# Kernel optimization log

Hardware: AMD Instinct MI355X
Metric: run time of the kernel (lower is better)

Reference implementation:

```python
import jax, jax.numpy as jnp
import numpy as np

B, N, K = 8, 2048, 16   # batch, points, neighbors (after dropping self)
EPS = 1e-5


def _bn(y, g, b, m, v):
    # eval-mode batchnorm over channel dim 1, y: [B,C,...]
    sh = (1, -1) + (1,) * (y.ndim - 2)
    inv = g.reshape(sh) / jnp.sqrt(v.reshape(sh) + EPS)
    return (y - m.reshape(sh)) * inv + b.reshape(sh)


def setup_inputs() -> dict:
    key = jax.random.key(0)
    ks = jax.random.split(key, 16)
    d = {}
    d["x"] = jax.random.normal(ks[0], (B, 3, N), dtype=jnp.float32)
    # pre: Conv1d(3->24, k=1) + BN
    d["w_pre"] = jax.random.normal(ks[1], (24, 3), dtype=jnp.float32) * 0.3
    d["b_pre"] = jax.random.normal(ks[2], (24,), dtype=jnp.float32) * 0.1
    d["g_pre"] = 1.0 + 0.1 * jax.random.normal(ks[3], (24,), dtype=jnp.float32)
    d["be_pre"] = 0.1 * jax.random.normal(ks[4], (24,), dtype=jnp.float32)
    d["m_pre"] = 0.1 * jax.random.normal(ks[5], (24,), dtype=jnp.float32)
    d["v_pre"] = jax.random.uniform(ks[6], (24,), minval=0.5, maxval=1.5, dtype=jnp.float32)
    # shared_mlp_1: Conv2d(48->12, 1, bias=False) + BN
    d["w1"] = jax.random.normal(ks[7], (12, 48), dtype=jnp.float32) * 0.15
    d["g1"] = 1.0 + 0.1 * jax.random.normal(ks[8], (12,), dtype=jnp.float32)
    d["be1"] = 0.1 * jax.random.normal(ks[9], (12,), dtype=jnp.float32)
    d["m1"] = 0.1 * jax.random.normal(ks[10], (12,), dtype=jnp.float32)
    d["v1"] = jax.random.uniform(ks[11], (12,), minval=0.5, maxval=1.5, dtype=jnp.float32)
    # shared_mlp_2: Conv2d(60->12, 1, bias=False) + BN
    d["w2"] = jax.random.normal(ks[12], (12, 60), dtype=jnp.float32) * 0.15
    d["g2"] = 1.0 + 0.1 * jax.random.normal(ks[13], (12,), dtype=jnp.float32)
    d["be2"] = 0.1 * jax.random.normal(ks[14], (12,), dtype=jnp.float32)
    d["m2"] = 0.1 * jax.random.normal(ks[15], (12,), dtype=jnp.float32)
    d["v2"] = jnp.ones((12,), dtype=jnp.float32)
    # shared_mlp_3: Conv2d(72->12, 1, bias=False), no BN
    d["w3"] = jax.random.normal(jax.random.fold_in(key, 99), (12, 72), dtype=jnp.float32) * 0.15
    return d


def reference(x, w_pre, b_pre, g_pre, be_pre, m_pre, v_pre,
              w1, g1, be1, m1, v1, w2, g2, be2, m2, v2, w3):
    # pre: 1x1 conv1d + BN + ReLU -> [B,24,N]
    pre = jnp.einsum('oc,bcn->bon', w_pre, x) + b_pre[None, :, None]
    pre = jax.nn.relu(_bn(pre, g_pre, be_pre, m_pre, v_pre))

    # kNN on xyz = x.detach(): [B,N,3]
    pts = jax.lax.stop_gradient(jnp.swapaxes(x, 1, 2))
    sq = jnp.sum(pts * pts, axis=-1)                              # [B,N]
    d2 = sq[:, :, None] + sq[:, None, :] - 2.0 * jnp.einsum('bnc,bmc->bnm', pts, pts)
    _, idx = jax.lax.top_k(-d2, K + 1)                             # nearest K+1 incl. self
    idx = idx[..., 1:]                                             # drop self -> [B,N,K]

    # gather neighbor features: [B,24,N,K]
    grouped = jax.vmap(lambda f, i: f[:, i])(pre, idx)
    center = jnp.broadcast_to(pre[..., None], grouped.shape)
    y = jnp.concatenate([center, grouped], axis=1)                 # [B,48,N,K]

    h1 = jax.nn.relu(_bn(jnp.einsum('oc,bcnk->bonk', w1, y), g1, be1, m1, v1))
    y = jnp.concatenate([h1, y], axis=1)                           # [B,60,N,K]
    h2 = jax.nn.relu(_bn(jnp.einsum('oc,bcnk->bonk', w2, y), g2, be2, m2, v2))
    y = jnp.concatenate([h2, y], axis=1)                           # [B,72,N,K]
    h3 = jnp.einsum('oc,bcnk->bonk', w3, y)
    y = jnp.concatenate([h3, y], axis=1)                           # [B,84,N,K]

    y = jnp.max(y, axis=-1)                                        # maxpool over neighbors -> [B,84,N]
    return jnp.concatenate([y, x], axis=1)                         # [B,87,N]
```

## Files before the change

### kernel.cpp

```cpp
#include <hip/hip_runtime.h>
#include <math.h>

#define EPS 1e-5f
#define NBATCH 8
#define NPTS 2048
#define KNB 16
#define BIG 3.2e38f

#define CHUNK_PTS 32
#define KNN_BLKS (NBATCH * 64)
#define THREADS 512
#define FUSED_LDS 49152

#define WS_PRE 0
#define WS_AUX (16384 * 24)
#define WS_IDX (WS_AUX + 16384 * 72)

__device__ __forceinline__ float dist2f(float mex, float mey, float mez,
                                        float sqn, float4 q) {
  float dot2 = fmaf(mex, q.x, fmaf(mey, q.y, __fmul_rn(mez, q.z)));
  return __fsub_rn(__fadd_rn(sqn, q.w), dot2);
}

template <bool HASSELF>
__device__ __forceinline__ void scan_slice(const float4* __restrict__ Cs, int selfc,
                                           float mex, float mey, float mez,
                                           float sqn, float L[16]) {
  for (int c0 = 0; c0 < 128; c0 += 16) {
    float S[16];
#pragma unroll
    for (int cc = 0; cc < 16; ++cc) {
      float4 q = Cs[c0 + cc];
      float d2 = dist2f(mex, mey, mez, sqn, q);
      if (HASSELF) S[cc] = ((c0 + cc) == selfc) ? BIG : d2;
      else         S[cc] = d2;
    }
#pragma unroll
    for (int pw = 1; pw < 16; pw <<= 1) {
#pragma unroll
      for (int k = pw; k >= 1; k >>= 1) {
#pragma unroll
        for (int j = (k & (pw - 1)); j + k < 16; j += 2 * k) {
#pragma unroll
          for (int i = 0; i < k; ++i) {
            int a = i + j, bq = i + j + k;
            if (bq < 16 && (a / (2 * pw) == bq / (2 * pw))) {
              float lo = fminf(S[a], S[bq]);
              float hi = fmaxf(S[a], S[bq]);
              S[a] = lo; S[bq] = hi;
            }
          }
        }
      }
    }
    float m[16];
#pragma unroll
    for (int i = 0; i < 16; ++i) m[i] = fminf(L[i], S[15 - i]);
#pragma unroll
    for (int d = 8; d >= 1; d >>= 1) {
#pragma unroll
      for (int i = 0; i < 16; ++i) {
        if (!(i & d)) {
          float lo = fminf(m[i], m[i | d]);
          float hi = fmaxf(m[i], m[i | d]);
          m[i] = lo; m[i | d] = hi;
        }
      }
    }
#pragma unroll
    for (int i = 0; i < 16; ++i) L[i] = m[i];
  }
}

__global__ __launch_bounds__(THREADS, 6) void fused_kernel(
    const float* __restrict__ x,
    const float* __restrict__ w_pre, const float* __restrict__ b_pre,
    const float* __restrict__ g_pre, const float* __restrict__ be_pre,
    const float* __restrict__ m_pre, const float* __restrict__ v_pre,
    const float* __restrict__ w1, const float* __restrict__ g1,
    const float* __restrict__ be1, const float* __restrict__ m1,
    const float* __restrict__ v1,
    const float* __restrict__ w2, const float* __restrict__ g2,
    const float* __restrict__ be2, const float* __restrict__ m2,
    const float* __restrict__ v2, const float* __restrict__ w3,
    float* __restrict__ pre, float* __restrict__ aux,
    int* __restrict__ knn_out) {
  extern __shared__ char smem[];
  float4* C4   = (float4*)smem;
  float* slist = (float*)(smem + 32768);
  float* fwp   = slist;
  float* fbp   = fwp + 72;
  float* fw1t  = fbp + 24;
  float* fb1   = fw1t + 576;
  float* fw2t  = fb1 + 12;
  float* fb2   = fw2t + 720;
  float* fw3t  = fb2 + 12;
  float* sinv1 = fw3t + 576;
  float* sinv2 = sinv1 + 12;
  float* sinvP = sinv2 + 12;
  float* sd2  = slist;
  int*   sidx = (int*)(slist + 640);
  int*   scnt = (int*)(slist + 1280);

  int tid = threadIdx.x;
  int bi = blockIdx.x;
  int b = bi >> 6, chunk = bi & 63;
  const float* xb = x + (size_t)b * 3 * NPTS;

  for (int j = tid; j < NPTS; j += THREADS) {
    float xx = xb[j], yy = xb[NPTS + j], zz = xb[2 * NPTS + j];
    float sq = __fadd_rn(__fadd_rn(__fmul_rn(xx, xx), __fmul_rn(yy, yy)),
                         __fmul_rn(zz, zz));
    C4[j] = make_float4(2.0f * xx, 2.0f * yy, 2.0f * zz, sq);
  }
  if (tid < 24) sinvP[tid] = g_pre[tid] / sqrtf(v_pre[tid] + EPS);
  if (tid < 12) { sinv1[tid] = g1[tid] / sqrtf(v1[tid] + EPS);
                  sinv2[tid] = g2[tid] / sqrtf(v2[tid] + EPS); }
  __syncthreads();
  if (tid < 72) fwp[tid] = w_pre[tid] * sinvP[tid / 3];
  if (tid < 24) fbp[tid] = (b_pre[tid] - m_pre[tid]) * sinvP[tid] + be_pre[tid];
  if (tid < 12) { fb1[tid] = be1[tid] - m1[tid] * sinv1[tid];
                  fb2[tid] = be2[tid] - m2[tid] * sinv2[tid]; }
  for (int j = tid; j < 576; j += THREADS) { int i = j / 12, o = j - i * 12; fw1t[j] = w1[o * 48 + i] * sinv1[o]; }
  for (int j = tid; j < 720; j += THREADS) { int i = j / 12, o = j - i * 12; fw2t[j] = w2[o * 60 + i] * sinv2[o]; }
  for (int j = tid; j < 576; j += THREADS) { int i = j / 12, o = j - i * 12; fw3t[j] = w3[o * 72 + 24 + i]; }
  __syncthreads();

  {
    int r = tid & 15, pt = tid >> 4;
    int n0 = chunk * CHUNK_PTS + pt;
    size_t pgl = (size_t)(b << 11) + n0;
    float x0 = xb[n0], x1 = xb[NPTS + n0], x2 = xb[2 * NPTS + n0];
    float pr[24];
#pragma unroll
    for (int c = 0; c < 24; ++c) {
      float v = fmaf(fwp[c * 3 + 0], x0,
                fmaf(fwp[c * 3 + 1], x1,
                fmaf(fwp[c * 3 + 2], x2, fbp[c])));
      pr[c] = fmaxf(v, 0.f);
    }
    if (r == 12) {
      float4* o4 = (float4*)(pre + pgl * 24);
#pragma unroll
      for (int i = 0; i < 6; ++i)
        o4[i] = make_float4(pr[4*i], pr[4*i+1], pr[4*i+2], pr[4*i+3]);
    }
    if (r < 12) {
      int o = r;
      float u1 = fb1[o], a1 = 0.f, u2 = fb2[o], a2 = 0.f, u3 = 0.f, a3 = 0.f;
#pragma unroll
      for (int i = 0; i < 24; ++i) {
        u1 = fmaf(fw1t[i * 12 + o],        pr[i], u1);
        a1 = fmaf(fw1t[(24 + i) * 12 + o], pr[i], a1);
        u2 = fmaf(fw2t[(12 + i) * 12 + o], pr[i], u2);
        a2 = fmaf(fw2t[(36 + i) * 12 + o], pr[i], a2);
        u3 = fmaf(fw3t[i * 12 + o],        pr[i], u3);
        a3 = fmaf(fw3t[(24 + i) * 12 + o], pr[i], a3);
      }
      float* A = aux + pgl * 72;
      A[o] = u1; A[12 + o] = u2; A[24 + o] = u3;
      A[36 + o] = a1; A[48 + o] = a2; A[60 + o] = a3;
    }
  }
  __syncthreads();

  int p = tid & 31, s = tid >> 5;
  int w = tid >> 6;
  int n = chunk * CHUNK_PTS + p;
  float4 me4 = C4[n];
  float mex = 0.5f * me4.x, mey = 0.5f * me4.y, mez = 0.5f * me4.z;
  float sqn = me4.w;
  const float4* Cs = C4 + s * 128;
  int selfc = n - s * 128;
  int wself = chunk >> 3;
  float L[16];
#pragma unroll
  for (int t = 0; t < 16; ++t) L[t] = BIG;
  if (w == wself) scan_slice<true >(Cs, selfc, mex, mey, mez, sqn, L);
  else            scan_slice<false>(Cs, selfc, mex, mey, mez, sqn, L);
  {
    float bb[16], m16[16];
#pragma unroll
    for (int i = 0; i < 16; ++i) bb[i] = __shfl_xor(L[i], 32, 64);
#pragma unroll
    for (int i = 0; i < 16; ++i) m16[i] = fminf(L[i], bb[15 - i]);
#pragma unroll
    for (int d = 8; d >= 1; d >>= 1) {
#pragma unroll
      for (int i = 0; i < 16; ++i) {
        if (!(i & d)) {
          float lo = fminf(m16[i], m16[i | d]);
          float hi = fmaxf(m16[i], m16[i | d]);
          m16[i] = lo; m16[i | d] = hi;
        }
      }
    }
    if (!(s & 1)) {
#pragma unroll
      for (int i = 0; i < 16; ++i) slist[(w * 16 + i) * 32 + p] = m16[i];
    }
  }
  __syncthreads();
  for (int W = 4; W >= 1; W >>= 1) {
    int u = tid >> 5;
    bool act = (u < W);
    float a[16], bb[16];
    if (act) {
#pragma unroll
      for (int i = 0; i < 16; ++i) a[i]  = slist[((2 * u) * 16 + i) * 32 + p];
#pragma unroll
      for (int i = 0; i < 16; ++i) bb[i] = slist[((2 * u + 1) * 16 + i) * 32 + p];
    }
    __syncthreads();
    if (act) {
      float m16[16];
#pragma unroll
      for (int i = 0; i < 16; ++i) m16[i] = fminf(a[i], bb[15 - i]);
#pragma unroll
      for (int d = 8; d >= 1; d >>= 1) {
#pragma unroll
        for (int i = 0; i < 16; ++i) {
          if (!(i & d)) {
            float lo = fminf(m16[i], m16[i | d]);
            float hi = fmaxf(m16[i], m16[i | d]);
            m16[i] = lo; m16[i | d] = hi;
          }
        }
      }
#pragma unroll
      for (int i = 0; i < 16; ++i) slist[(u * 16 + i) * 32 + p] = m16[i];
    }
    __syncthreads();
  }
  float tau = slist[15 * 32 + p];
  __syncthreads();
  for (int j = tid; j < 32 * 20; j += THREADS) sidx[j] = 0;
  if (tid < 32) scnt[tid] = 0;
  __syncthreads();
  if (w == wself) {
#pragma unroll 4
    for (int c = 0; c < 128; ++c) {
      float4 q = Cs[c];
      float d2 = dist2f(mex, mey, mez, sqn, q);
      int j = s * 128 + c;
      if (d2 <= tau && j != n) {
        int pos = atomicAdd(&scnt[p], 1);
        if (pos < 20) { sd2[p * 20 + pos] = d2; sidx[p * 20 + pos] = j; }
      }
    }
  } else {
#pragma unroll 4
    for (int c = 0; c < 128; ++c) {
      float4 q = Cs[c];
      float d2 = dist2f(mex, mey, mez, sqn, q);
      int j = s * 128 + c;
      if (d2 <= tau) {
        int pos = atomicAdd(&scnt[p], 1);
        if (pos < 20) { sd2[p * 20 + pos] = d2; sidx[p * 20 + pos] = j; }
      }
    }
  }
  __syncthreads();
  if (tid < 32) {
    int c = scnt[tid]; if (c > 20) c = 20;
    if (c > 16) {
      for (int t = 0; t < 16; ++t) {
        int best = t;
        for (int u = t + 1; u < c; ++u) {
          float da = sd2[tid * 20 + u], db = sd2[tid * 20 + best];
          int ia = sidx[tid * 20 + u], ib = sidx[tid * 20 + best];
          if (da < db || (da == db && ia < ib)) best = u;
        }
        float td = sd2[tid * 20 + t]; sd2[tid * 20 + t] = sd2[tid * 20 + best]; sd2[tid * 20 + best] = td;
        int ti = sidx[tid * 20 + t]; sidx[tid * 20 + t] = sidx[tid * 20 + best]; sidx[tid * 20 + best] = ti;
      }
    }
  }
  __syncthreads();
  {
    int pp = tid >> 4, kk = tid & 15;
    knn_out[((size_t)b * NPTS + chunk * CHUNK_PTS + pp) * KNB + kk] = sidx[pp * 20 + kk];
  }
}

__global__ __launch_bounds__(256) void mlp_kernel(
    const float* __restrict__ pre, const float* __restrict__ aux,
    const int* __restrict__ knn, const float* __restrict__ x,
    const float* __restrict__ w2, const float* __restrict__ g2,
    const float* __restrict__ v2, const float* __restrict__ w3,
    float* __restrict__ out) {
  __shared__ float sW2h[144], sW3h2[144], sW3h1[144];
  __shared__ float sout[87 * 16];
  int tid = threadIdx.x;
  if (tid < 144) {
    int o = tid / 12, i = tid - o * 12;
    float inv2 = g2[o] / sqrtf(v2[o] + EPS);
    sW2h[tid]  = w2[o * 60 + i] * inv2;
    sW3h2[tid] = w3[o * 72 + i];
    sW3h1[tid] = w3[o * 72 + 12 + i];
  }
  __syncthreads();
  int k = tid & 15, pl = tid >> 4;
  int p = blockIdx.x * 16 + pl;
  int b = p >> 11, n = p & (NPTS - 1);
  int nb = knn[(size_t)p * KNB + k];
  const float4* u4 = (const float4*)(aux + (size_t)p * 72);
  const float4* a4 = (const float4*)(aux + ((size_t)(b << 11) + nb) * 72 + 36);
  float uc[36], av[36];
#pragma unroll
  for (int i = 0; i < 9; ++i) {
    float4 t = u4[i];
    uc[4*i] = t.x; uc[4*i+1] = t.y; uc[4*i+2] = t.z; uc[4*i+3] = t.w;
    float4 t2 = a4[i];
    av[4*i] = t2.x; av[4*i+1] = t2.y; av[4*i+2] = t2.z; av[4*i+3] = t2.w;
  }
  float h1[12], h2[12], h3[12];
#pragma unroll
  for (int o = 0; o < 12; ++o) h1[o] = fmaxf(uc[o] + av[o], 0.f);
#pragma unroll
  for (int o = 0; o < 12; ++o) {
    float a = uc[12 + o] + av[12 + o];
#pragma unroll
    for (int i = 0; i < 12; ++i) a = fmaf(sW2h[o * 12 + i], h1[i], a);
    h2[o] = fmaxf(a, 0.f);
  }
#pragma unroll
  for (int o = 0; o < 12; ++o) {
    float a = uc[24 + o] + av[24 + o];
#pragma unroll
    for (int i = 0; i < 12; ++i) a = fmaf(sW3h2[o * 12 + i], h2[i], a);
#pragma unroll
    for (int i = 0; i < 12; ++i) a = fmaf(sW3h1[o * 12 + i], h1[i], a);
    h3[o] = a;
  }
  float nbf[24];
  const float4* pn4 = (const float4*)(pre + ((size_t)(b << 11) + nb) * 24);
#pragma unroll
  for (int i = 0; i < 6; ++i) {
    float4 t = pn4[i];
    nbf[4*i] = t.x; nbf[4*i+1] = t.y; nbf[4*i+2] = t.z; nbf[4*i+3] = t.w;
  }
#pragma unroll
  for (int m = 1; m < 16; m <<= 1) {
#pragma unroll
    for (int o = 0; o < 12; ++o) {
      h1[o] = fmaxf(h1[o], __shfl_xor(h1[o], m, 16));
      h2[o] = fmaxf(h2[o], __shfl_xor(h2[o], m, 16));
      h3[o] = fmaxf(h3[o], __shfl_xor(h3[o], m, 16));
    }
#pragma unroll
    for (int i = 0; i < 24; ++i)
      nbf[i] = fmaxf(nbf[i], __shfl_xor(nbf[i], m, 16));
  }
  if (k == 0) {
    const float4* c4 = (const float4*)(pre + (size_t)p * 24);
#pragma unroll
    for (int o = 0; o < 12; ++o) {
      sout[(0  + o) * 16 + pl] = h3[o];
      sout[(12 + o) * 16 + pl] = h2[o];
      sout[(24 + o) * 16 + pl] = h1[o];
    }
#pragma unroll
    for (int i = 0; i < 6; ++i) {
      float4 t = c4[i];
      sout[(36 + 4*i    ) * 16 + pl] = t.x;
      sout[(36 + 4*i + 1) * 16 + pl] = t.y;
      sout[(36 + 4*i + 2) * 16 + pl] = t.z;
      sout[(36 + 4*i + 3) * 16 + pl] = t.w;
    }
#pragma unroll
    for (int i = 0; i < 24; ++i) sout[(60 + i) * 16 + pl] = nbf[i];
    const float* xb = x + (size_t)b * 3 * NPTS + n;
    sout[84 * 16 + pl] = xb[0];
    sout[85 * 16 + pl] = xb[NPTS];
    sout[86 * 16 + pl] = xb[2 * NPTS];
  }
  __syncthreads();
  int n0 = (blockIdx.x * 16) & (NPTS - 1);
  float* ob = out + (size_t)b * 87 * NPTS;
  for (int j2 = tid; j2 < 87 * 16; j2 += 256) {
    int c = j2 >> 4, i = j2 & 15;
    ob[(size_t)c * NPTS + n0 + i] = sout[j2];
  }
}

extern "C" void kernel_launch(void* const* d_in, const int* in_sizes, int n_in,
                              void* d_out, int out_size, void* d_ws, size_t ws_size,
                              hipStream_t stream) {
  (void)in_sizes; (void)n_in; (void)out_size; (void)ws_size;
  const float* x     = (const float*)d_in[0];
  const float* w_pre = (const float*)d_in[1];
  const float* b_pre = (const float*)d_in[2];
  const float* g_pre = (const float*)d_in[3];
  const float* be_pre= (const float*)d_in[4];
  const float* m_pre = (const float*)d_in[5];
  const float* v_pre = (const float*)d_in[6];
  const float* w1    = (const float*)d_in[7];
  const float* g1    = (const float*)d_in[8];
  const float* be1   = (const float*)d_in[9];
  const float* m1    = (const float*)d_in[10];
  const float* v1    = (const float*)d_in[11];
  const float* w2    = (const float*)d_in[12];
  const float* g2    = (const float*)d_in[13];
  const float* be2   = (const float*)d_in[14];
  const float* m2    = (const float*)d_in[15];
  const float* v2    = (const float*)d_in[16];
  const float* w3    = (const float*)d_in[17];
  float* ws  = (float*)d_ws;
  float* pre = ws + WS_PRE;
  float* aux = ws + WS_AUX;
  int*   knn = (int*)(ws + WS_IDX);
  float* out = (float*)d_out;

  fused_kernel<<<KNN_BLKS, THREADS, FUSED_LDS, stream>>>(
      x, w_pre, b_pre, g_pre, be_pre, m_pre, v_pre,
      w1, g1, be1, m1, v1, w2, g2, be2, m2, v2, w3,
      pre, aux, knn);
  mlp_kernel<<<NBATCH * NPTS / 16, 256, 0, stream>>>(pre, aux, knn, x,
                                                     w2, g2, v2, w3, out);
}
```

Before: 151.5 us.

## Halve KNN block to 16 points, add in-wave two-level merge and LDS swizzle

Shrinks each fused block from 32 points with 512 threads to 16 points with 256 threads, doubling the grid so that more blocks run concurrently. The first stage of the top-16 merge now uses two in-wave shuffle steps (xor 16, then xor 32) instead of an LDS round trip. Each group of 16 threads reads the candidate slice in an XOR-rotated order, which spreads broadcast LDS reads across banks. The distance is rewritten with negated coordinates so it becomes a single FMA chain, which can change rounding slightly relative to the reference. The work in the unseen later part of the kernel must still match the new chunk size.

```diff
diff --git a/kernel.cpp b/kernel.cpp
--- a/kernel.cpp
+++ b/kernel.cpp
@@ -7,10 +7,10 @@
 #define KNB 16
 #define BIG 3.2e38f
 
-#define CHUNK_PTS 32
-#define KNN_BLKS (NBATCH * 64)
-#define THREADS 512
-#define FUSED_LDS 49152
+#define CHUNK_PTS 16
+#define KNN_BLKS (NBATCH * 128)
+#define THREADS 256
+#define FUSED_LDS 40960
 
 #define WS_PRE 0
 #define WS_AUX (16384 * 24)
@@ -18,21 +18,21 @@
 
 __device__ __forceinline__ float dist2f(float mex, float mey, float mez,
                                         float sqn, float4 q) {
-  float dot2 = fmaf(mex, q.x, fmaf(mey, q.y, __fmul_rn(mez, q.z)));
-  return __fsub_rn(__fadd_rn(sqn, q.w), dot2);
+  return fmaf(mex, q.x, fmaf(mey, q.y, fmaf(mez, q.z, __fadd_rn(sqn, q.w))));
 }
 
 template <bool HASSELF>
 __device__ __forceinline__ void scan_slice(const float4* __restrict__ Cs, int selfc,
-                                           float mex, float mey, float mez,
+                                           int rot, float mex, float mey, float mez,
                                            float sqn, float L[16]) {
   for (int c0 = 0; c0 < 128; c0 += 16) {
     float S[16];
 #pragma unroll
     for (int cc = 0; cc < 16; ++cc) {
-      float4 q = Cs[c0 + cc];
+      int c2 = (c0 + cc) ^ rot;
+      float4 q = Cs[c2];
       float d2 = dist2f(mex, mey, mez, sqn, q);
-      if (HASSELF) S[cc] = ((c0 + cc) == selfc) ? BIG : d2;
+      if (HASSELF) S[cc] = (c2 == selfc) ? BIG : d2;
       else         S[cc] = d2;
     }
 #pragma unroll
@@ -72,7 +72,7 @@
   }
 }
 
-__global__ __launch_bounds__(THREADS, 6) void fused_kernel(
+__global__ __launch_bounds__(THREADS, 4) void fused_kernel(
     const float* __restrict__ x,
     const float* __restrict__ w_pre, const float* __restrict__ b_pre,
     const float* __restrict__ g_pre, const float* __restrict__ be_pre,
@@ -99,19 +99,19 @@
   float* sinv2 = sinv1 + 12;
   float* sinvP = sinv2 + 12;
   float* sd2  = slist;
-  int*   sidx = (int*)(slist + 640);
-  int*   scnt = (int*)(slist + 1280);
+  int*   sidx = (int*)(slist + 320);
+  int*   scnt = (int*)(slist + 640);
 
   int tid = threadIdx.x;
   int bi = blockIdx.x;
-  int b = bi >> 6, chunk = bi & 63;
+  int b = bi >> 7, chunk = bi & 127;
   const float* xb = x + (size_t)b * 3 * NPTS;
 
   for (int j = tid; j < NPTS; j += THREADS) {
     float xx = xb[j], yy = xb[NPTS + j], zz = xb[2 * NPTS + j];
     float sq = __fadd_rn(__fadd_rn(__fmul_rn(xx, xx), __fmul_rn(yy, yy)),
                          __fmul_rn(zz, zz));
-    C4[j] = make_float4(2.0f * xx, 2.0f * yy, 2.0f * zz, sq);
+    C4[j] = make_float4(-2.0f * xx, -2.0f * yy, -2.0f * zz, sq);
   }
   if (tid < 24) sinvP[tid] = g_pre[tid] / sqrtf(v_pre[tid] + EPS);
   if (tid < 12) { sinv1[tid] = g1[tid] / sqrtf(v1[tid] + EPS);
@@ -164,24 +164,25 @@
   }
   __syncthreads();
 
-  int p = tid & 31, s = tid >> 5;
+  int p = tid & 15, s = tid >> 4;
   int w = tid >> 6;
   int n = chunk * CHUNK_PTS + p;
   float4 me4 = C4[n];
-  float mex = 0.5f * me4.x, mey = 0.5f * me4.y, mez = 0.5f * me4.z;
+  float mex = -0.5f * me4.x, mey = -0.5f * me4.y, mez = -0.5f * me4.z;
   float sqn = me4.w;
   const float4* Cs = C4 + s * 128;
   int selfc = n - s * 128;
-  int wself = chunk >> 3;
+  int rot = (s & 3) << 1;
+  int wself = chunk >> 5;
   float L[16];
 #pragma unroll
   for (int t = 0; t < 16; ++t) L[t] = BIG;
-  if (w == wself) scan_slice<true >(Cs, selfc, mex, mey, mez, sqn, L);
-  else            scan_slice<false>(Cs, selfc, mex, mey, mez, sqn, L);
+  if (w == wself) scan_slice<true >(Cs, selfc, rot, mex, mey, mez, sqn, L);
+  else            scan_slice<false>(Cs, selfc, rot, mex, mey, mez, sqn, L);
   {
     float bb[16], m16[16];
 #pragma unroll
-    for (int i = 0; i < 16; ++i) bb[i] = __shfl_xor(L[i], 32, 64);
+    for (int i = 0; i < 16; ++i) bb[i] = __shfl_xor(L[i], 16, 64);
 #pragma unroll
     for (int i = 0; i < 16; ++i) m16[i] = fminf(L[i], bb[15 - i]);
 #pragma unroll
@@ -195,21 +196,37 @@
         }
       }
     }
-    if (!(s & 1)) {
-#pragma unroll
-      for (int i = 0; i < 16; ++i) slist[(w * 16 + i) * 32 + p] = m16[i];
-    }
-  }
-  __syncthreads();
-  for (int W = 4; W >= 1; W >>= 1) {
-    int u = tid >> 5;
+#pragma unroll
+    for (int i = 0; i < 16; ++i) bb[i] = __shfl_xor(m16[i], 32, 64);
+    float m2_[16];
+#pragma unroll
+    for (int i = 0; i < 16; ++i) m2_[i] = fminf(m16[i], bb[15 - i]);
+#pragma unroll
+    for (int d = 8; d >= 1; d >>= 1) {
+#pragma unroll
+      for (int i = 0; i < 16; ++i) {
+        if (!(i & d)) {
+          float lo = fminf(m2_[i], m2_[i | d]);
+          float hi = fmaxf(m2_[i], m2_[i | d]);
+          m2_[i] = lo; m2_[i | d] = hi;
+        }
+      }
+    }
+    if ((s & 3) == 0) {
+#pragma unroll
+      for (int i = 0; i < 16; ++i) slist[(w * 16 + i) * 16 + p] = m2_[i];
+    }
+  }
+  __syncthreads();
+  for (int W = 2; W >= 1; W >>= 1) {
+    int u = tid >> 4;
     bool act = (u < W);
     float a[16], bb[16];
     if (act) {
 #pragma unroll
-      for (int i = 0; i < 16; ++i) a[i]  = slist[((2 * u) * 16 + i) * 32 + p];
-#pragma unroll
-      for (int i = 0; i < 16; ++i) bb[i] = slist[((2 * u + 1) * 16 + i) * 32 + p];
+      for (int i = 0; i < 16; ++i) a[i]  = slist[((2 * u) * 16 + i) * 16 + p];
+#pragma unroll
+      for (int i = 0; i < 16; ++i) bb[i] = slist[((2 * u + 1) * 16 + i) * 16 + p];
     }
     __syncthreads();
     if (act) {
@@ -228,21 +245,22 @@
         }
       }
 #pragma unroll
-      for (int i = 0; i < 16; ++i) slist[(u * 16 + i) * 32 + p] = m16[i];
+      for (int i = 0; i < 16; ++i) slist[(u * 16 + i) * 16 + p] = m16[i];
     }
     __syncthreads();
   }
-  float tau = slist[15 * 32 + p];
-  __syncthreads();
-  for (int j = tid; j < 32 * 20; j += THREADS) sidx[j] = 0;
-  if (tid < 32) scnt[tid] = 0;
+  float tau = slist[15 * 16 + p];
+  __syncthreads();
+  for (int j = tid; j < 16 * 20; j += THREADS) sidx[j] = 0;
+  if (tid < 16) scnt[tid] = 0;
   __syncthreads();
   if (w == wself) {
 #pragma unroll 4
     for (int c = 0; c < 128; ++c) {
-      float4 q = Cs[c];
+      int c2 = c ^ rot;
+      float4 q = Cs[c2];
       float d2 = dist2f(mex, mey, mez, sqn, q);
-      int j = s * 128 + c;
+      int j = s * 128 + c2;
       if (d2 <= tau && j != n) {
         int pos = atomicAdd(&scnt[p], 1);
         if (pos < 20) { sd2[p * 20 + pos] = d2; sidx[p * 20 + pos] = j; }
@@ -251,9 +269,10 @@
   } else {
 #pragma unroll 4
     for (int c = 0; c < 128; ++c) {
-      float4 q = Cs[c];
+      int c2 = c ^ rot;
+      float4 q = Cs[c2];
       float d2 = dist2f(mex, mey, mez, sqn, q);
-      int j = s * 128 + c;
+      int j = s * 128 + c2;
       if (d2 <= tau) {
         int pos = atomicAdd(&scnt[p], 1);
         if (pos < 20) { sd2[p * 20 + pos] = d2; sidx[p * 20 + pos] = j; }
@@ -261,7 +280,7 @@
     }
   }
   __syncthreads();
-  if (tid < 32) {
+  if (tid < 16) {
     int c = scnt[tid]; if (c > 20) c = 20;
     if (c > 16) {
       for (int t = 0; t < 16; ++t) {
```

Result: slower. 158.6 us (+4.7%).

## Remap KNN threads so top-16 merge happens within a wavefront via shuffles

Applied to the files above, without the earlier changes.

Threads are remapped so each wavefront owns 4 query points across 16 candidate slices, letting the per-point top-16 merge run entirely through xor-shuffles instead of a multi-round LDS tree reduction with several block barriers. The self-exclusion template split is removed and the distance is folded into a single fma chain using negated coordinates. Scratch buffers get their own LDS region, so their zeroing moves earlier and the LDS size shrinks. Launch bounds drop from 6 to 4 blocks per CU, which gives more registers per thread but may lower occupancy; removing the barrier after the MLP stage relies on the new LDS layout not overlapping the weights.

```diff
diff --git a/kernel.cpp b/kernel.cpp
--- a/kernel.cpp
+++ b/kernel.cpp
@@ -10,7 +10,7 @@
 #define CHUNK_PTS 32
 #define KNN_BLKS (NBATCH * 64)
 #define THREADS 512
-#define FUSED_LDS 49152
+#define FUSED_LDS 46176
 
 #define WS_PRE 0
 #define WS_AUX (16384 * 24)
@@ -18,61 +18,10 @@
 
 __device__ __forceinline__ float dist2f(float mex, float mey, float mez,
                                         float sqn, float4 q) {
-  float dot2 = fmaf(mex, q.x, fmaf(mey, q.y, __fmul_rn(mez, q.z)));
-  return __fsub_rn(__fadd_rn(sqn, q.w), dot2);
+  return fmaf(mex, q.x, fmaf(mey, q.y, fmaf(mez, q.z, __fadd_rn(sqn, q.w))));
 }
 
-template <bool HASSELF>
-__device__ __forceinline__ void scan_slice(const float4* __restrict__ Cs, int selfc,
-                                           float mex, float mey, float mez,
-                                           float sqn, float L[16]) {
-  for (int c0 = 0; c0 < 128; c0 += 16) {
-    float S[16];
-#pragma unroll
-    for (int cc = 0; cc < 16; ++cc) {
-      float4 q = Cs[c0 + cc];
-      float d2 = dist2f(mex, mey, mez, sqn, q);
-      if (HASSELF) S[cc] = ((c0 + cc) == selfc) ? BIG : d2;
-      else         S[cc] = d2;
-    }
-#pragma unroll
-    for (int pw = 1; pw < 16; pw <<= 1) {
-#pragma unroll
-      for (int k = pw; k >= 1; k >>= 1) {
-#pragma unroll
-        for (int j = (k & (pw - 1)); j + k < 16; j += 2 * k) {
-#pragma unroll
-          for (int i = 0; i < k; ++i) {
-            int a = i + j, bq = i + j + k;
-            if (bq < 16 && (a / (2 * pw) == bq / (2 * pw))) {
-              float lo = fminf(S[a], S[bq]);
-              float hi = fmaxf(S[a], S[bq]);
-              S[a] = lo; S[bq] = hi;
-            }
-          }
-        }
-      }
-    }
-    float m[16];
-#pragma unroll
-    for (int i = 0; i < 16; ++i) m[i] = fminf(L[i], S[15 - i]);
-#pragma unroll
-    for (int d = 8; d >= 1; d >>= 1) {
-#pragma unroll
-      for (int i = 0; i < 16; ++i) {
-        if (!(i & d)) {
-          float lo = fminf(m[i], m[i | d]);
-          float hi = fmaxf(m[i], m[i | d]);
-          m[i] = lo; m[i | d] = hi;
-        }
-      }
-    }
-#pragma unroll
-    for (int i = 0; i < 16; ++i) L[i] = m[i];
-  }
-}
-
-__global__ __launch_bounds__(THREADS, 6) void fused_kernel(
+__global__ __launch_bounds__(THREADS, 4) void fused_kernel(
     const float* __restrict__ x,
     const float* __restrict__ w_pre, const float* __restrict__ b_pre,
     const float* __restrict__ g_pre, const float* __restrict__ be_pre,
@@ -86,9 +35,9 @@
     float* __restrict__ pre, float* __restrict__ aux,
     int* __restrict__ knn_out) {
   extern __shared__ char smem[];
-  float4* C4   = (float4*)smem;
-  float* slist = (float*)(smem + 32768);
-  float* fwp   = slist;
+  float4* C4  = (float4*)smem;
+  float* wreg = (float*)(smem + 32768);
+  float* fwp   = wreg;
   float* fbp   = fwp + 72;
   float* fw1t  = fbp + 24;
   float* fb1   = fw1t + 576;
@@ -98,9 +47,9 @@
   float* sinv1 = fw3t + 576;
   float* sinv2 = sinv1 + 12;
   float* sinvP = sinv2 + 12;
-  float* sd2  = slist;
-  int*   sidx = (int*)(slist + 640);
-  int*   scnt = (int*)(slist + 1280);
+  float* sd2  = (float*)(smem + 40928);
+  int*   sidx = (int*)(smem + 43488);
+  int*   scnt = (int*)(smem + 46048);
 
   int tid = threadIdx.x;
   int bi = blockIdx.x;
@@ -111,8 +60,10 @@
     float xx = xb[j], yy = xb[NPTS + j], zz = xb[2 * NPTS + j];
     float sq = __fadd_rn(__fadd_rn(__fmul_rn(xx, xx), __fmul_rn(yy, yy)),
                          __fmul_rn(zz, zz));
-    C4[j] = make_float4(2.0f * xx, 2.0f * yy, 2.0f * zz, sq);
-  }
+    C4[j] = make_float4(-2.0f * xx, -2.0f * yy, -2.0f * zz, sq);
+  }
+  for (int j = tid; j < 32 * 20; j += THREADS) sidx[j] = 0;
+  if (tid < 32) scnt[tid] = 0;
   if (tid < 24) sinvP[tid] = g_pre[tid] / sqrtf(v_pre[tid] + EPS);
   if (tid < 12) { sinv1[tid] = g1[tid] / sqrtf(v1[tid] + EPS);
                   sinv2[tid] = g2[tid] / sqrtf(v2[tid] + EPS); }
@@ -162,26 +113,68 @@
       A[36 + o] = a1; A[48 + o] = a2; A[60 + o] = a3;
     }
   }
-  __syncthreads();
-
-  int p = tid & 31, s = tid >> 5;
+
+  int l = tid & 63;
   int w = tid >> 6;
+  int p = (w << 2) | (l & 3);
+  int s = l >> 2;
   int n = chunk * CHUNK_PTS + p;
   float4 me4 = C4[n];
-  float mex = 0.5f * me4.x, mey = 0.5f * me4.y, mez = 0.5f * me4.z;
+  float mex = -0.5f * me4.x, mey = -0.5f * me4.y, mez = -0.5f * me4.z;
   float sqn = me4.w;
   const float4* Cs = C4 + s * 128;
   int selfc = n - s * 128;
-  int wself = chunk >> 3;
   float L[16];
 #pragma unroll
   for (int t = 0; t < 16; ++t) L[t] = BIG;
-  if (w == wself) scan_slice<true >(Cs, selfc, mex, mey, mez, sqn, L);
-  else            scan_slice<false>(Cs, selfc, mex, mey, mez, sqn, L);
-  {
+  for (int c0 = 0; c0 < 128; c0 += 16) {
+    float S[16];
+#pragma unroll
+    for (int cc = 0; cc < 16; ++cc) {
+      float4 q = Cs[c0 + cc];
+      float d2 = dist2f(mex, mey, mez, sqn, q);
+      S[cc] = ((c0 + cc) == selfc) ? BIG : d2;
+    }
+#pragma unroll
+    for (int pw = 1; pw < 16; pw <<= 1) {
+#pragma unroll
+      for (int k = pw; k >= 1; k >>= 1) {
+#pragma unroll
+        for (int j = (k & (pw - 1)); j + k < 16; j += 2 * k) {
+#pragma unroll
+          for (int i = 0; i < k; ++i) {
+            int a = i + j, bq = i + j + k;
+            if (bq < 16 && (a / (2 * pw) == bq / (2 * pw))) {
+              float lo = fminf(S[a], S[bq]);
+              float hi = fmaxf(S[a], S[bq]);
+              S[a] = lo; S[bq] = hi;
+            }
+          }
+        }
+      }
+    }
+    float m[16];
+#pragma unroll
+    for (int i = 0; i < 16; ++i) m[i] = fminf(L[i], S[15 - i]);
+#pragma unroll
+    for (int d = 8; d >= 1; d >>= 1) {
+#pragma unroll
+      for (int i = 0; i < 16; ++i) {
+        if (!(i & d)) {
+          float lo = fminf(m[i], m[i | d]);
+          float hi = fmaxf(m[i], m[i | d]);
+          m[i] = lo; m[i | d] = hi;
+        }
+      }
+    }
+#pragma unroll
+    for (int i = 0; i < 16; ++i) L[i] = m[i];
+  }
+#pragma unroll
+  for (int mk = 4; mk <= 32; mk <<= 1) {
     float bb[16], m16[16];
 #pragma unroll
-    for (int i = 0; i < 16; ++i) bb[i] = __shfl_xor(L[i], 32, 64);
+    for (int i = 0; i < 16; ++i) bb[i] = __shfl_xor(L[i], mk, 64);
 #pragma unroll
     for (int i = 0; i < 16; ++i) m16[i] = fminf(L[i], bb[15 - i]);
 #pragma unroll
@@ -195,69 +188,18 @@
         }
       }
     }
-    if (!(s & 1)) {
-#pragma unroll
-      for (int i = 0; i < 16; ++i) slist[(w * 16 + i) * 32 + p] = m16[i];
-    }
-  }
-  __syncthreads();
-  for (int W = 4; W >= 1; W >>= 1) {
-    int u = tid >> 5;
-    bool act = (u < W);
-    float a[16], bb[16];
-    if (act) {
-#pragma unroll
-      for (int i = 0; i < 16; ++i) a[i]  = slist[((2 * u) * 16 + i) * 32 + p];
-#pragma unroll
-      for (int i = 0; i < 16; ++i) bb[i] = slist[((2 * u + 1) * 16 + i) * 32 + p];
-    }
-    __syncthreads();
-    if (act) {
-      float m16[16];
-#pragma unroll
-      for (int i = 0; i < 16; ++i) m16[i] = fminf(a[i], bb[15 - i]);
-#pragma unroll
-      for (int d = 8; d >= 1; d >>= 1) {
-#pragma unroll
-        for (int i = 0; i < 16; ++i) {
-          if (!(i & d)) {
-            float lo = fminf(m16[i], m16[i | d]);
-            float hi = fmaxf(m16[i], m16[i | d]);
-            m16[i] = lo; m16[i | d] = hi;
-          }
-        }
-      }
-#pragma unroll
-      for (int i = 0; i < 16; ++i) slist[(u * 16 + i) * 32 + p] = m16[i];
-    }
-    __syncthreads();
-  }
-  float tau = slist[15 * 32 + p];
-  __syncthreads();
-  for (int j = tid; j < 32 * 20; j += THREADS) sidx[j] = 0;
-  if (tid < 32) scnt[tid] = 0;
-  __syncthreads();
-  if (w == wself) {
+#pragma unroll
+    for (int i = 0; i < 16; ++i) L[i] = m16[i];
+  }
+  float tau = L[15];
 #pragma unroll 4
-    for (int c = 0; c < 128; ++c) {
-      float4 q = Cs[c];
-      float d2 = dist2f(mex, mey, mez, sqn, q);
-      int j = s * 128 + c;
-      if (d2 <= tau && j != n) {
-        int pos = atomicAdd(&scnt[p], 1);
-        if (pos < 20) { sd2[p * 20 + pos] = d2; sidx[p * 20 + pos] = j; }
-      }
-    }
-  } else {
-#pragma unroll 4
-    for (int c = 0; c < 128; ++c) {
-      float4 q = Cs[c];
-      float d2 = dist2f(mex, mey, mez, sqn, q);
-      int j = s * 128 + c;
-      if (d2 <= tau) {
-        int pos = atomicAdd(&scnt[p], 1);
-        if (pos < 20) { sd2[p * 20 + pos] = d2; sidx[p * 20 + pos] = j; }
-      }
+  for (int c = 0; c < 128; ++c) {
+    float4 q = Cs[c];
+    float d2 = dist2f(mex, mey, mez, sqn, q);
+    int j = s * 128 + c;
+    if (d2 <= tau && j != n) {
+      int pos = atomicAdd(&scnt[p], 1);
+      if (pos < 20) { sd2[p * 20 + pos] = d2; sidx[p * 20 + pos] = j; }
     }
   }
   __syncthreads();
```

Result: slower. 159.9 us (+5.5%).

## Sort points by x and search KNN in a local window with fallback

Applied to the files above, without the earlier changes.

A new kernel bitonic-sorts each batch's points by x coordinate. The KNN kernel then scans only a window of 768 sorted neighbours around each query instead of all 2048 points. It checks whether the x-gap to the window edges could hide a closer point and, if so, falls back to the full scan from global memory. This cuts distance computations and shared-memory footprint, at the cost of an extra sort launch, a mapping of indices back to original order, and a slower path for blocks that need the fallback.

```diff
diff --git a/kernel.cpp b/kernel.cpp
--- a/kernel.cpp
+++ b/kernel.cpp
@@ -10,65 +10,103 @@
 #define CHUNK_PTS 32
 #define KNN_BLKS (NBATCH * 64)
 #define THREADS 512
-#define FUSED_LDS 49152
+#define HALF 384
+#define WMAX 832
+#define FUSED_LDS 38304
 
 #define WS_PRE 0
-#define WS_AUX (16384 * 24)
-#define WS_IDX (WS_AUX + 16384 * 72)
-
-__device__ __forceinline__ float dist2f(float mex, float mey, float mez,
-                                        float sqn, float4 q) {
-  float dot2 = fmaf(mex, q.x, fmaf(mey, q.y, __fmul_rn(mez, q.z)));
-  return __fsub_rn(__fadd_rn(sqn, q.w), dot2);
-}
-
-template <bool HASSELF>
-__device__ __forceinline__ void scan_slice(const float4* __restrict__ Cs, int selfc,
-                                           float mex, float mey, float mez,
-                                           float sqn, float L[16]) {
-  for (int c0 = 0; c0 < 128; c0 += 16) {
-    float S[16];
-#pragma unroll
-    for (int cc = 0; cc < 16; ++cc) {
-      float4 q = Cs[c0 + cc];
-      float d2 = dist2f(mex, mey, mez, sqn, q);
-      if (HASSELF) S[cc] = ((c0 + cc) == selfc) ? BIG : d2;
-      else         S[cc] = d2;
-    }
-#pragma unroll
-    for (int pw = 1; pw < 16; pw <<= 1) {
-#pragma unroll
-      for (int k = pw; k >= 1; k >>= 1) {
-#pragma unroll
-        for (int j = (k & (pw - 1)); j + k < 16; j += 2 * k) {
-#pragma unroll
-          for (int i = 0; i < k; ++i) {
-            int a = i + j, bq = i + j + k;
-            if (bq < 16 && (a / (2 * pw) == bq / (2 * pw))) {
-              float lo = fminf(S[a], S[bq]);
-              float hi = fmaxf(S[a], S[bq]);
-              S[a] = lo; S[bq] = hi;
-            }
+#define WS_AUX 393216
+#define WS_IDX 1572864
+#define WS_SX4 1835008
+#define WS_SID 1900544
+
+__device__ __forceinline__ float dist2f(float mex, float mey, float mez, float sqn,
+                                        float qx, float qy, float qz, float qw) {
+  return fmaf(mex, qx, fmaf(mey, qy, fmaf(mez, qz, __fadd_rn(sqn, qw))));
+}
+
+__device__ __forceinline__ void sort16(float S[16]) {
+#pragma unroll
+  for (int pw = 1; pw < 16; pw <<= 1) {
+#pragma unroll
+    for (int k = pw; k >= 1; k >>= 1) {
+#pragma unroll
+      for (int j = (k & (pw - 1)); j + k < 16; j += 2 * k) {
+#pragma unroll
+        for (int i = 0; i < k; ++i) {
+          int a = i + j, bq = i + j + k;
+          if (bq < 16 && (a / (2 * pw) == bq / (2 * pw))) {
+            float lo = fminf(S[a], S[bq]);
+            float hi = fmaxf(S[a], S[bq]);
+            S[a] = lo; S[bq] = hi;
           }
         }
       }
     }
-    float m[16];
-#pragma unroll
-    for (int i = 0; i < 16; ++i) m[i] = fminf(L[i], S[15 - i]);
-#pragma unroll
-    for (int d = 8; d >= 1; d >>= 1) {
-#pragma unroll
-      for (int i = 0; i < 16; ++i) {
-        if (!(i & d)) {
-          float lo = fminf(m[i], m[i | d]);
-          float hi = fmaxf(m[i], m[i | d]);
-          m[i] = lo; m[i | d] = hi;
-        }
-      }
-    }
-#pragma unroll
-    for (int i = 0; i < 16; ++i) L[i] = m[i];
+  }
+}
+
+__device__ __forceinline__ void clean16(float m[16]) {
+#pragma unroll
+  for (int d = 8; d >= 1; d >>= 1) {
+#pragma unroll
+    for (int i = 0; i < 16; ++i) {
+      if (!(i & d)) {
+        float lo = fminf(m[i], m[i | d]);
+        float hi = fmaxf(m[i], m[i | d]);
+        m[i] = lo; m[i | d] = hi;
+      }
+    }
+  }
+}
+
+__device__ __forceinline__ void merge16(float L[16], const float S[16]) {
+  float m[16];
+#pragma unroll
+  for (int i = 0; i < 16; ++i) m[i] = fminf(L[i], S[15 - i]);
+  clean16(m);
+#pragma unroll
+  for (int i = 0; i < 16; ++i) L[i] = m[i];
+}
+
+__device__ __forceinline__ void shflmerge16(float L[16], int mask) {
+  float bb[16], m[16];
+#pragma unroll
+  for (int i = 0; i < 16; ++i) bb[i] = __shfl_xor(L[i], mask, 64);
+#pragma unroll
+  for (int i = 0; i < 16; ++i) m[i] = fminf(L[i], bb[15 - i]);
+  clean16(m);
+#pragma unroll
+  for (int i = 0; i < 16; ++i) L[i] = m[i];
+}
+
+__global__ __launch_bounds__(1024) void sort_kernel(
+    const float* __restrict__ x, float* __restrict__ sx4g, int* __restrict__ sidxg) {
+  __shared__ float kx[NPTS];
+  __shared__ int ki[NPTS];
+  int b = blockIdx.x, tid = threadIdx.x;
+  const float* xb = x + (size_t)b * 3 * NPTS;
+  for (int j = tid; j < NPTS; j += 1024) { kx[j] = xb[j]; ki[j] = j; }
+  __syncthreads();
+  for (int k = 2; k <= NPTS; k <<= 1) {
+    for (int j = k >> 1; j > 0; j >>= 1) {
+      int t = 2 * tid - (tid & (j - 1));
+      int t2 = t | j;
+      bool up = ((t & k) == 0);
+      float a = kx[t], c = kx[t2];
+      int ia = ki[t], ic = ki[t2];
+      bool sw = up ? (a > c) : (a < c);
+      if (sw) { kx[t] = c; kx[t2] = a; ki[t] = ic; ki[t2] = ia; }
+      __syncthreads();
+    }
+  }
+  for (int j = tid; j < NPTS; j += 1024) {
+    int n = ki[j];
+    float xx = kx[j], yy = xb[NPTS + n], zz = xb[2 * NPTS + n];
+    float sq = __fadd_rn(__fadd_rn(__fmul_rn(xx, xx), __fmul_rn(yy, yy)),
+                         __fmul_rn(zz, zz));
+    ((float4*)sx4g)[(b << 11) + j] = make_float4(-2.0f * xx, -2.0f * yy, -2.0f * zz, sq);
+    sidxg[(b << 11) + j] = n;
   }
 }
 
@@ -83,12 +121,14 @@
     const float* __restrict__ w2, const float* __restrict__ g2,
     const float* __restrict__ be2, const float* __restrict__ m2,
     const float* __restrict__ v2, const float* __restrict__ w3,
+    const float* __restrict__ sx4g, const int* __restrict__ sidxg,
     float* __restrict__ pre, float* __restrict__ aux,
     int* __restrict__ knn_out) {
   extern __shared__ char smem[];
-  float4* C4   = (float4*)smem;
-  float* slist = (float*)(smem + 32768);
-  float* fwp   = slist;
+  float2* Wxy = (float2*)smem;
+  float2* Wzs = (float2*)(smem + 6656);
+  int*   Widx = (int*)(smem + 13312);
+  float* fwp   = (float*)(smem + 16640);
   float* fbp   = fwp + 72;
   float* fw1t  = fbp + 24;
   float* fb1   = fw1t + 576;
@@ -98,21 +138,36 @@
   float* sinv1 = fw3t + 576;
   float* sinv2 = sinv1 + 12;
   float* sinvP = sinv2 + 12;
-  float* sd2  = slist;
-  int*   sidx = (int*)(slist + 640);
-  int*   scnt = (int*)(slist + 1280);
+  float* slist = (float*)(smem + 16640);
+  float* sd2   = (float*)(smem + 33024);
+  int*   sidxT = (int*)(smem + 35584);
+  int*   scnt  = (int*)(smem + 38144);
+  int*   sflag = (int*)(smem + 38272);
 
   int tid = threadIdx.x;
   int bi = blockIdx.x;
   int b = bi >> 6, chunk = bi & 63;
+  int bq = b << 11;
+  int vlo = chunk * CHUNK_PTS - HALF;
   const float* xb = x + (size_t)b * 3 * NPTS;
-
-  for (int j = tid; j < NPTS; j += THREADS) {
-    float xx = xb[j], yy = xb[NPTS + j], zz = xb[2 * NPTS + j];
-    float sq = __fadd_rn(__fadd_rn(__fmul_rn(xx, xx), __fmul_rn(yy, yy)),
-                         __fmul_rn(zz, zz));
-    C4[j] = make_float4(2.0f * xx, 2.0f * yy, 2.0f * zz, sq);
-  }
+  const float4* sx4 = (const float4*)sx4g;
+
+  for (int idx = tid; idx < WMAX; idx += THREADS) {
+    int g = vlo + idx;
+    if ((unsigned)g < (unsigned)NPTS) {
+      float4 f = sx4[bq + g];
+      Wxy[idx] = make_float2(f.x, f.y);
+      Wzs[idx] = make_float2(f.z, f.w);
+      Widx[idx] = sidxg[bq + g];
+    } else {
+      Wxy[idx] = make_float2(0.f, 0.f);
+      Wzs[idx] = make_float2(0.f, BIG);
+      Widx[idx] = 0;
+    }
+  }
+  for (int j = tid; j < 32 * 20; j += THREADS) sidxT[j] = 0;
+  if (tid < 32) scnt[tid] = 0;
+  if (tid == 32) *sflag = 0;
   if (tid < 24) sinvP[tid] = g_pre[tid] / sqrtf(v_pre[tid] + EPS);
   if (tid < 12) { sinv1[tid] = g1[tid] / sqrtf(v1[tid] + EPS);
                   sinv2[tid] = g2[tid] / sqrtf(v2[tid] + EPS); }
@@ -128,8 +183,8 @@
 
   {
     int r = tid & 15, pt = tid >> 4;
-    int n0 = chunk * CHUNK_PTS + pt;
-    size_t pgl = (size_t)(b << 11) + n0;
+    int n0 = sidxg[bq + chunk * CHUNK_PTS + pt];
+    size_t pgl = (size_t)bq + n0;
     float x0 = xb[n0], x1 = xb[NPTS + n0], x2 = xb[2 * NPTS + n0];
     float pr[24];
 #pragma unroll
@@ -165,40 +220,32 @@
   __syncthreads();
 
   int p = tid & 31, s = tid >> 5;
-  int w = tid >> 6;
-  int n = chunk * CHUNK_PTS + p;
-  float4 me4 = C4[n];
-  float mex = 0.5f * me4.x, mey = 0.5f * me4.y, mez = 0.5f * me4.z;
-  float sqn = me4.w;
-  const float4* Cs = C4 + s * 128;
-  int selfc = n - s * 128;
-  int wself = chunk >> 3;
+  int q = chunk * CHUNK_PTS + p;
+  float2 mxy = Wxy[p + HALF], mzs = Wzs[p + HALF];
+  float mex = -0.5f * mxy.x, mey = -0.5f * mxy.y, mez = -0.5f * mzs.x;
+  float sqn = mzs.y;
   float L[16];
 #pragma unroll
   for (int t = 0; t < 16; ++t) L[t] = BIG;
-  if (w == wself) scan_slice<true >(Cs, selfc, mex, mey, mez, sqn, L);
-  else            scan_slice<false>(Cs, selfc, mex, mey, mez, sqn, L);
-  {
-    float bb[16], m16[16];
-#pragma unroll
-    for (int i = 0; i < 16; ++i) bb[i] = __shfl_xor(L[i], 32, 64);
-#pragma unroll
-    for (int i = 0; i < 16; ++i) m16[i] = fminf(L[i], bb[15 - i]);
-#pragma unroll
-    for (int d = 8; d >= 1; d >>= 1) {
-#pragma unroll
-      for (int i = 0; i < 16; ++i) {
-        if (!(i & d)) {
-          float lo = fminf(m16[i], m16[i | d]);
-          float hi = fmaxf(m16[i], m16[i | d]);
-          m16[i] = lo; m16[i | d] = hi;
-        }
-      }
-    }
-    if (!(s & 1)) {
-#pragma unroll
-      for (int i = 0; i < 16; ++i) slist[(w * 16 + i) * 32 + p] = m16[i];
-    }
+#pragma unroll
+  for (int t = 0; t < 3; ++t) {
+    float S[16];
+#pragma unroll
+    for (int cc = 0; cc < 16; ++cc) {
+      int idx = p + s * 16 + t * 256 + cc;
+      float2 a = Wxy[idx], z = Wzs[idx];
+      float d2 = dist2f(mex, mey, mez, sqn, a.x, a.y, z.x, z.y);
+      if (t * 256 + cc == 256) d2 = (s == 8) ? BIG : d2;
+      S[cc] = d2;
+    }
+    sort16(S);
+    merge16(L, S);
+  }
+  shflmerge16(L, 32);
+  if (!(s & 1)) {
+    int w = tid >> 6;
+#pragma unroll
+    for (int i = 0; i < 16; ++i) slist[(w * 16 + i) * 32 + p] = L[i];
   }
   __syncthreads();
   for (int W = 4; W >= 1; W >>= 1) {
@@ -213,50 +260,98 @@
     }
     __syncthreads();
     if (act) {
-      float m16[16];
-#pragma unroll
-      for (int i = 0; i < 16; ++i) m16[i] = fminf(a[i], bb[15 - i]);
-#pragma unroll
-      for (int d = 8; d >= 1; d >>= 1) {
-#pragma unroll
-        for (int i = 0; i < 16; ++i) {
-          if (!(i & d)) {
-            float lo = fminf(m16[i], m16[i | d]);
-            float hi = fmaxf(m16[i], m16[i | d]);
-            m16[i] = lo; m16[i | d] = hi;
-          }
+      float m[16];
+#pragma unroll
+      for (int i = 0; i < 16; ++i) m[i] = fminf(a[i], bb[15 - i]);
+      clean16(m);
+#pragma unroll
+      for (int i = 0; i < 16; ++i) slist[(u * 16 + i) * 32 + p] = m[i];
+    }
+    __syncthreads();
+  }
+  float tau = slist[15 * 32 + p];
+  if (tid < 32) {
+    int qq = chunk * CHUNK_PTS + tid;
+    float xq = -0.5f * Wxy[tid + HALF].x;
+    float tt = slist[15 * 32 + tid];
+    bool bad = false;
+    int gl = qq - HALF - 1;
+    if (gl >= 0) { float xe = -0.5f * sx4[bq + gl].x; float dx = xe - xq; if (dx * dx <= tt) bad = true; }
+    int gr = qq + HALF;
+    if (gr < NPTS) { float xe = -0.5f * sx4[bq + gr].x; float dx = xe - xq; if (dx * dx <= tt) bad = true; }
+    if (bad) atomicOr(sflag, 1);
+  }
+  __syncthreads();
+  int flag = *sflag;
+
+  if (!flag) {
+#pragma unroll
+    for (int t = 0; t < 3; ++t) {
+#pragma unroll
+      for (int cc = 0; cc < 16; ++cc) {
+        int idx = p + s * 16 + t * 256 + cc;
+        float2 a = Wxy[idx], z = Wzs[idx];
+        float d2 = dist2f(mex, mey, mez, sqn, a.x, a.y, z.x, z.y);
+        bool self = (t * 256 + cc == 256) && (s == 8);
+        if (!self && d2 <= tau) {
+          int pos = atomicAdd(&scnt[p], 1);
+          if (pos < 20) { sd2[p * 20 + pos] = d2; sidxT[p * 20 + pos] = Widx[idx]; }
         }
       }
-#pragma unroll
-      for (int i = 0; i < 16; ++i) slist[(u * 16 + i) * 32 + p] = m16[i];
+    }
+  } else {
+    const float4* Cg = sx4 + bq + s * 128;
+    float L2[16];
+#pragma unroll
+    for (int t = 0; t < 16; ++t) L2[t] = BIG;
+    for (int c0 = 0; c0 < 128; c0 += 16) {
+      float S[16];
+#pragma unroll
+      for (int cc = 0; cc < 16; ++cc) {
+        float4 f = Cg[c0 + cc];
+        float d2 = dist2f(mex, mey, mez, sqn, f.x, f.y, f.z, f.w);
+        int gg = s * 128 + c0 + cc;
+        S[cc] = (gg == q) ? BIG : d2;
+      }
+      sort16(S);
+      merge16(L2, S);
+    }
+    shflmerge16(L2, 32);
+    if (!(s & 1)) {
+      int w = tid >> 6;
+#pragma unroll
+      for (int i = 0; i < 16; ++i) slist[(w * 16 + i) * 32 + p] = L2[i];
     }
     __syncthreads();
-  }
-  float tau = slist[15 * 32 + p];
-  __syncthreads();
-  for (int j = tid; j < 32 * 20; j += THREADS) sidx[j] = 0;
-  if (tid < 32) scnt[tid] = 0;
-  __syncthreads();
-  if (w == wself) {
-#pragma unroll 4
+    for (int W = 4; W >= 1; W >>= 1) {
+      int u = tid >> 5;
+      bool act = (u < W);
+      float a[16], bb[16];
+      if (act) {
+#pragma unroll
+        for (int i = 0; i < 16; ++i) a[i]  = slist[((2 * u) * 16 + i) * 32 + p];
+#pragma unroll
+        for (int i = 0; i < 16; ++i) bb[i] = slist[((2 * u + 1) * 16 + i) * 32 + p];
+      }
+      __syncthreads();
+      if (act) {
+        float m[16];
+#pragma unroll
+        for (int i = 0; i < 16; ++i) m[i] = fminf(a[i], bb[15 - i]);
+        clean16(m);
+#pragma unroll
+        for (int i = 0; i < 16; ++i) slist[(u * 16 + i) * 32 + p] = m[i];
+      }
+      __syncthreads();
+    }
+    float tau2 = slist[15 * 32 + p];
     for (int c = 0; c < 128; ++c) {
-      float4 q = Cs[c];
-      float d2 = dist2f(mex, mey, mez, sqn, q);
-      int j = s * 128 + c;
-      if (d2 <= tau && j != n) {
+      float4 f = Cg[c];
+      float d2 = dist2f(mex, mey, mez, sqn, f.x, f.y, f.z, f.w);
+      int gg = s * 128 + c;
+      if (gg != q && d2 <= tau2) {
         int pos = atomicAdd(&scnt[p], 1);
-        if (pos < 20) { sd2[p * 20 + pos] = d2; sidx[p * 20 + pos] = j; }
-      }
-    }
-  } else {
-#pragma unroll 4
-    for (int c = 0; c < 128; ++c) {
-      float4 q = Cs[c];
-      float d2 = dist2f(mex, mey, mez, sqn, q);
-      int j = s * 128 + c;
-      if (d2 <= tau) {
-        int pos = atomicAdd(&scnt[p], 1);
-        if (pos < 20) { sd2[p * 20 + pos] = d2; sidx[p * 20 + pos] = j; }
+        if (pos < 20) { sd2[p * 20 + pos] = d2; sidxT[p * 20 + pos] = sidxg[bq + gg]; }
       }
     }
   }
@@ -268,18 +363,19 @@
         int best = t;
         for (int u = t + 1; u < c; ++u) {
           float da = sd2[tid * 20 + u], db = sd2[tid * 20 + best];
-          int ia = sidx[tid * 20 + u], ib = sidx[tid * 20 + best];
+          int ia = sidxT[tid * 20 + u], ib = sidxT[tid * 20 + best];
           if (da < db || (da == db && ia < ib)) best = u;
         }
         float td = sd2[tid * 20 + t]; sd2[tid * 20 + t] = sd2[tid * 20 + best]; sd2[tid * 20 + best] = td;
-        int ti = sidx[tid * 20 + t]; sidx[tid * 20 + t] = sidx[tid * 20 + best]; sidx[tid * 20 + best] = ti;
+        int ti = sidxT[tid * 20 + t]; sidxT[tid * 20 + t] = sidxT[tid * 20 + best]; sidxT[tid * 20 + best] = ti;
       }
     }
   }
   __syncthreads();
   {
     int pp = tid >> 4, kk = tid & 15;
-    knn_out[((size_t)b * NPTS + chunk * CHUNK_PTS + pp) * KNB + kk] = sidx[pp * 20 + kk];
+    int n_orig = sidxg[bq + chunk * CHUNK_PTS + pp];
+    knn_out[((size_t)b * NPTS + n_orig) * KNB + kk] = sidxT[pp * 20 + kk];
   }
 }
 
@@ -406,16 +502,19 @@
   const float* m2    = (const float*)d_in[15];
   const float* v2    = (const float*)d_in[16];
   const float* w3    = (const float*)d_in[17];
-  float* ws  = (float*)d_ws;
-  float* pre = ws + WS_PRE;
-  float* aux = ws + WS_AUX;
-  int*   knn = (int*)(ws + WS_IDX);
-  float* out = (float*)d_out;
-
+  float* ws   = (float*)d_ws;
+  float* pre  = ws + WS_PRE;
+  float* aux  = ws + WS_AUX;
+  int*   knn  = (int*)(ws + WS_IDX);
+  float* sx4g = ws + WS_SX4;
+  int*  sidxg = (int*)(ws + WS_SID);
+  float* out  = (float*)d_out;
+
+  sort_kernel<<<NBATCH, 1024, 0, stream>>>(x, sx4g, sidxg);
   fused_kernel<<<KNN_BLKS, THREADS, FUSED_LDS, stream>>>(
       x, w_pre, b_pre, g_pre, be_pre, m_pre, v_pre,
       w1, g1, be1, m1, v1, w2, g2, be2, m2, v2, w3,
-      pre, aux, knn);
+      sx4g, sidxg, pre, aux, knn);
   mlp_kernel<<<NBATCH * NPTS / 16, 256, 0, stream>>>(pre, aux, knn, x,
                                                      w2, g2, v2, w3, out);
 }
```

New measurement: 203.2 us. 34.1% more time.
